# Optimization experiments

Measured on AMD Instinct MI355X. Metric: run time of the kernel, lower is better.

## Reference

```python
import jax, jax.numpy as jnp
import numpy as np

C_MSA, C_PAIR, C = 64, 128, 32


def setup_inputs() -> dict:
    key = jax.random.key(0)
    ks = jax.random.split(key, 7)
    n_msa, n_token = 512, 384
    msa = jax.random.normal(ks[0], (n_msa, n_token, C_MSA), dtype=jnp.float32)
    gamma = jnp.ones((C_MSA,), dtype=jnp.float32)
    beta = jnp.zeros((C_MSA,), dtype=jnp.float32)
    # nn.Linear weights are [out, in]
    w_a = jax.random.normal(ks[1], (C, C_MSA), dtype=jnp.float32) * (1.0 / np.sqrt(C_MSA))
    w_b = jax.random.normal(ks[2], (C, C_MSA), dtype=jnp.float32) * (1.0 / np.sqrt(C_MSA))
    w_out = jax.random.normal(ks[3], (C_PAIR, C * C), dtype=jnp.float32) * (1.0 / np.sqrt(C * C))
    b_out = jax.random.normal(ks[4], (C_PAIR,), dtype=jnp.float32) * 0.01
    return {"msa": msa, "gamma": gamma, "beta": beta, "w_a": w_a, "w_b": w_b,
            "w_out": w_out, "b_out": b_out}


def _layernorm(x, gamma, beta, eps=1e-5):
    mu = jnp.mean(x, axis=-1, keepdims=True)
    var = jnp.mean(jnp.square(x - mu), axis=-1, keepdims=True)
    return (x - mu) * jax.lax.rsqrt(var + eps) * gamma + beta


def reference(msa, gamma, beta, w_a, w_b, w_out, b_out):
    # msa: [S, I, c_msa]
    n_msa = msa.shape[0]
    m = _layernorm(msa, gamma, beta)
    a = jnp.einsum('sic,dc->sid', m, w_a)  # [S, I, C]
    b = jnp.einsum('sic,dc->sid', m, w_b)  # [S, I, C]
    # outer product mean over MSA dim as a single GEMM-style contraction
    o = jnp.einsum('sic,sjd->ijcd', a, b) / n_msa  # [I, J, C, C]
    n_token = o.shape[0]
    o_flat = o.reshape(n_token, n_token, C * C)
    z = jnp.einsum('ijk,pk->ijp', o_flat, w_out) + b_out  # [I, J, c_pair]
    return z
```

## Files before the change

kernel.cpp:

```cpp
#include <hip/hip_runtime.h>
#include <hip/hip_bf16.h>
#include <stdint.h>

#define S_DIM 512
#define I_DIM 384
#define CMSA  64
#define CDIM  32
#define M_DIM (I_DIM*CDIM)
#define P_DIM 128

typedef __attribute__((ext_vector_type(8))) short  s16x8;
typedef __attribute__((ext_vector_type(8))) __bf16 bf16x8;
typedef __attribute__((ext_vector_type(4))) float  f32x4;

static __device__ __forceinline__ unsigned short f2bf(float f) {
  union { float f; unsigned u; } v; v.f = f;
  unsigned r = v.u + 0x7FFFu + ((v.u >> 16) & 1u);
  return (unsigned short)(r >> 16);
}

static __device__ __forceinline__ void gload_lds16(const void* g, void* l) {
  __builtin_amdgcn_global_load_lds(
      (__attribute__((address_space(1))) void*)(g),
      (__attribute__((address_space(3))) void*)(l), 16, 0, 0);
}

__global__ __launch_bounds__(256) void ln_proj_kernel(
    const float* __restrict__ msa, const float* __restrict__ gamma,
    const float* __restrict__ beta, const float* __restrict__ w_a,
    const float* __restrict__ w_b, unsigned short* __restrict__ Ag,
    unsigned short* __restrict__ Bg)
{
  __shared__ float wl[2][32][64];
  __shared__ float gb[2][64];
  __shared__ unsigned short atr[2][32][64];

  const int tid = threadIdx.x;
  float* wflat = &wl[0][0][0];
  for (int t = tid; t < 2048; t += 256) { wflat[t] = w_a[t]; wflat[2048 + t] = w_b[t]; }
  if (tid < 64) { gb[0][tid] = gamma[tid]; gb[1][tid] = beta[tid]; }
  __syncthreads();

  const int q = tid & 3, sl = tid >> 2;
  const int s = blockIdx.x * 64 + sl;
  const int i = blockIdx.y;
  const float* row = msa + ((size_t)s * I_DIM + i) * CMSA + q * 16;

  float x[16];
  #pragma unroll
  for (int u = 0; u < 4; ++u) {
    float4 v = *(const float4*)(row + 4*u);
    x[4*u] = v.x; x[4*u+1] = v.y; x[4*u+2] = v.z; x[4*u+3] = v.w;
  }
  float sum = 0.f, sq = 0.f;
  #pragma unroll
  for (int j = 0; j < 16; ++j) { sum += x[j]; sq += x[j]*x[j]; }
  sum += __shfl_xor(sum, 1); sum += __shfl_xor(sum, 2);
  sq  += __shfl_xor(sq, 1);  sq  += __shfl_xor(sq, 2);
  const float mean = sum * (1.f/64.f);
  const float var  = sq  * (1.f/64.f) - mean*mean;
  const float rstd = rsqrtf(var + 1e-5f);
  float m[16];
  #pragma unroll
  for (int j = 0; j < 16; ++j)
    m[j] = (x[j] - mean) * rstd * gb[0][q*16+j] + gb[1][q*16+j];

  for (int c = 0; c < 32; ++c) {
    float pa = 0.f, pb = 0.f;
    #pragma unroll
    for (int u = 0; u < 4; ++u) {
      float4 wa = *(const float4*)&wl[0][c][q*16 + 4*u];
      float4 wb = *(const float4*)&wl[1][c][q*16 + 4*u];
      pa += m[4*u]*wa.x + m[4*u+1]*wa.y + m[4*u+2]*wa.z + m[4*u+3]*wa.w;
      pb += m[4*u]*wb.x + m[4*u+1]*wb.y + m[4*u+2]*wb.z + m[4*u+3]*wb.w;
    }
    pa += __shfl_xor(pa, 1); pa += __shfl_xor(pa, 2);
    pb += __shfl_xor(pb, 1); pb += __shfl_xor(pb, 2);
    if (q == 0) {
      atr[0][c][sl] = f2bf(pa * (1.f/512.f));
      atr[1][c][sl] = f2bf(pb);
    }
  }
  __syncthreads();
  const int c2 = tid >> 3, su = (tid & 7) * 8;
  const size_t gbase = ((size_t)i * CDIM + c2) * S_DIM + (size_t)blockIdx.x * 64 + su;
  *(s16x8*)(Ag + gbase) = *(const s16x8*)&atr[0][c2][su];
  *(s16x8*)(Bg + gbase) = *(const s16x8*)&atr[1][c2][su];
}

__global__ __launch_bounds__(256) void wconv_kernel(
    const float* __restrict__ w, unsigned short* __restrict__ wp)
{
  const int idx = blockIdx.x * 256 + threadIdx.x;
  const int p = idx >> 10, k = idx & 1023;
  const int c = k >> 5, d = k & 31;
  wp[p*1024 + d*32 + c] = f2bf(w[idx]);
}

__global__ __launch_bounds__(512, 2) void opm_gemm_kernel(
    const unsigned short* __restrict__ Ag, const unsigned short* __restrict__ Bg,
    const unsigned short* __restrict__ Wp, const float* __restrict__ b_out,
    float* __restrict__ z)
{
  __shared__ __align__(16) unsigned char lds[131072];

  const int tid = threadIdx.x;
  const int l = tid & 63, w = tid >> 6;
  const int wr = w >> 2, wc = w & 3;

  const int bid = blockIdx.x;
  const int xcd = bid & 7, local = bid >> 3;
  const int bn = local / 6;
  const int bm = xcd * 6 + (local % 6);

  const unsigned short* pA[4];
  const unsigned short* pB[4];
  int u16[4];
  #pragma unroll
  for (int it = 0; it < 4; ++it) {
    const int u = it*512 + tid;
    const int r = u >> 3, slot = u & 7;
    const int ks8 = slot ^ (r & 7);
    pA[it] = Ag + ((size_t)(bm*256 + r))*S_DIM + ks8*8;
    pB[it] = Bg + ((size_t)(bn*256 + r))*S_DIM + ks8*8;
    u16[it] = u * 16;
  }

  int a_base[8], b_base[4];
  #pragma unroll
  for (int mi = 0; mi < 8; ++mi) {
    const int rowA = wr*128 + mi*16 + (l & 15);
    a_base[mi] = rowA*128 + ((((l >> 4)) ^ (rowA & 7)) << 4);
  }
  #pragma unroll
  for (int ni = 0; ni < 4; ++ni) {
    const int rowB = wc*64 + ni*16 + (l & 15);
    b_base[ni] = 65536 + rowB*128 + ((((l >> 4)) ^ (rowB & 7)) << 4);
  }

  f32x4 acc[8][4];
  #pragma unroll
  for (int a = 0; a < 8; ++a)
    #pragma unroll
    for (int b = 0; b < 4; ++b)
      acc[a][b] = (f32x4){0.f, 0.f, 0.f, 0.f};

  #pragma unroll
  for (int it = 0; it < 4; ++it) {
    gload_lds16(pA[it], lds + u16[it]);
    gload_lds16(pB[it], lds + 65536 + u16[it]);
    pA[it] += 64; pB[it] += 64;
  }
  __syncthreads();

  int cur = 0;
  for (int kt = 0; kt < 8; ++kt) {
    if (kt < 7) {
      const int nb = (cur ^ 1) * 32768;
      #pragma unroll
      for (int it = 0; it < 4; ++it) {
        gload_lds16(pA[it], lds + nb + u16[it]);
        gload_lds16(pB[it], lds + 65536 + nb + u16[it]);
        pA[it] += 64; pB[it] += 64;
      }
    }
    const int cb = cur * 32768;
    #pragma unroll
    for (int ks = 0; ks < 2; ++ks) {
      bf16x8 af[8], bf[4];
      const int kx = ks << 6;
      #pragma unroll
      for (int mi = 0; mi < 8; ++mi)
        af[mi] = *(const bf16x8*)(lds + cb + (a_base[mi] ^ kx));
      #pragma unroll
      for (int ni = 0; ni < 4; ++ni)
        bf[ni] = *(const bf16x8*)(lds + cb + (b_base[ni] ^ kx));
      __builtin_amdgcn_s_setprio(1);
      #pragma unroll
      for (int mi = 0; mi < 8; ++mi)
        #pragma unroll
        for (int ni = 0; ni < 4; ++ni)
          acc[mi][ni] = __builtin_amdgcn_mfma_f32_16x16x32_bf16(
              af[mi], bf[ni], acc[mi][ni], 0, 0, 0);
      __builtin_amdgcn_s_setprio(0);
    }
    __syncthreads();
    cur ^= 1;
  }

  #pragma unroll
  for (int mi = 0; mi < 8; ++mi) {
    const int iloc = wr*4 + (mi >> 1);
    const int cb2 = (mi & 1)*16 + (l >> 4)*4;
    #pragma unroll
    for (int ni = 0; ni < 4; ++ni) {
      const int jloc = wc*2 + (ni >> 1);
      const int d = (ni & 1)*16 + (l & 15);
      const int pair = iloc*8 + jloc;
      #pragma unroll
      for (int rp = 0; rp < 2; ++rp) {
        const int kp = d*32 + cb2 + 2*rp;
        int byte = pair*2048 + kp*2;
        byte ^= ((pair & 7) << 4) ^ (((byte >> 7) & 7) << 4);
        unsigned int val = (unsigned int)f2bf(acc[mi][ni][2*rp])
                         | ((unsigned int)f2bf(acc[mi][ni][2*rp+1]) << 16);
        *(unsigned int*)(lds + byte) = val;
      }
    }
  }
  __syncthreads();

  const unsigned short* wrow = Wp + ((size_t)(w*16 + (l & 15)))*1024 + (l >> 4)*8;
  f32x4 accz[4];
  #pragma unroll
  for (int ni = 0; ni < 4; ++ni) accz[ni] = (f32x4){0.f,0.f,0.f,0.f};

  #pragma unroll 4
  for (int ksp = 0; ksp < 32; ++ksp) {
    const bf16x8 wf = *(const bf16x8*)(wrow + ksp*32);
    const int kbyte = ksp*64 + (l >> 4)*16;
    const int kswz = ((kbyte >> 7) & 7) << 4;
    #pragma unroll
    for (int ni = 0; ni < 4; ++ni) {
      const int pair = ni*16 + (l & 15);
      int byte = pair*2048 + kbyte;
      byte ^= ((pair & 7) << 4) ^ kswz;
      const bf16x8 of = *(const bf16x8*)(lds + byte);
      accz[ni] = __builtin_amdgcn_mfma_f32_16x16x32_bf16(wf, of, accz[ni], 0, 0, 0);
    }
  }

  const int p0 = w*16 + (l >> 4)*4;
  const float4 bo = *(const float4*)(b_out + p0);
  #pragma unroll
  for (int ni = 0; ni < 4; ++ni) {
    const int pair = ni*16 + (l & 15);
    const int gi = bm*8 + (pair >> 3), gj = bn*8 + (pair & 7);
    float4 v;
    v.x = accz[ni][0] + bo.x; v.y = accz[ni][1] + bo.y;
    v.z = accz[ni][2] + bo.z; v.w = accz[ni][3] + bo.w;
    *(float4*)(z + ((size_t)gi * I_DIM + gj) * P_DIM + p0) = v;
  }
}

extern "C" void kernel_launch(void* const* d_in, const int* in_sizes, int n_in,
                              void* d_out, int out_size, void* d_ws, size_t ws_size,
                              hipStream_t stream) {
  const float* msa   = (const float*)d_in[0];
  const float* gamma = (const float*)d_in[1];
  const float* beta  = (const float*)d_in[2];
  const float* w_a   = (const float*)d_in[3];
  const float* w_b   = (const float*)d_in[4];
  const float* w_out = (const float*)d_in[5];
  const float* b_out = (const float*)d_in[6];
  float* z = (float*)d_out;

  unsigned short* Ag = (unsigned short*)d_ws;
  unsigned short* Bg = Ag + (size_t)M_DIM * S_DIM;
  unsigned short* Wp = Bg + (size_t)M_DIM * S_DIM;

  hipLaunchKernelGGL(ln_proj_kernel, dim3(8, 384), dim3(256), 0, stream,
                     msa, gamma, beta, w_a, w_b, Ag, Bg);
  hipLaunchKernelGGL(wconv_kernel, dim3(512), dim3(256), 0, stream, w_out, Wp);
  hipLaunchKernelGGL(opm_gemm_kernel, dim3(2304), dim3(512), 0, stream,
                     Ag, Bg, Wp, b_out, z);
}
```

Before: 369.0 us.

## Restructure LN-projection kernel and split GEMM prefetch with explicit vmcnt waits

The layernorm/projection kernel is rewritten so that each lane holds one output channel's weight row in registers. Each wave processes rows with a full-wave shuffle reduction, and results are packed as bf16 pairs into a swizzled LDS transpose buffer before vectorized stores. This avoids the LDS weight staging and the 32-iteration serial loop over channels. In the GEMM main loop, the next tile's global-to-LDS loads are split into two halves issued around the first k-substep. Explicit s_waitcnt vmcnt and raw barriers replace __syncthreads so loads overlap MFMA work, at the cost of extra barriers per iteration.

```diff
diff --git a/kernel.cpp b/kernel.cpp
--- a/kernel.cpp
+++ b/kernel.cpp
@@ -25,67 +25,84 @@
       (__attribute__((address_space(3))) void*)(l), 16, 0, 0);
 }
 
+#define VMCNT4() asm volatile("s_waitcnt vmcnt(4)" ::: "memory")
+#define VMCNT0() asm volatile("s_waitcnt vmcnt(0)" ::: "memory")
+#define BAR()    do { __builtin_amdgcn_s_barrier(); asm volatile("" ::: "memory"); } while (0)
+
 __global__ __launch_bounds__(256) void ln_proj_kernel(
     const float* __restrict__ msa, const float* __restrict__ gamma,
     const float* __restrict__ beta, const float* __restrict__ w_a,
     const float* __restrict__ w_b, unsigned short* __restrict__ Ag,
     unsigned short* __restrict__ Bg)
 {
-  __shared__ float wl[2][32][64];
-  __shared__ float gb[2][64];
-  __shared__ unsigned short atr[2][32][64];
+  __shared__ float mraw[4][64];
+  __shared__ unsigned int atr[64][32];
 
   const int tid = threadIdx.x;
-  float* wflat = &wl[0][0][0];
-  for (int t = tid; t < 2048; t += 256) { wflat[t] = w_a[t]; wflat[2048 + t] = w_b[t]; }
-  if (tid < 64) { gb[0][tid] = gamma[tid]; gb[1][tid] = beta[tid]; }
+  const int l = tid & 63, w = tid >> 6;
+  const int c = l & 31, h = l >> 5;
+  const int i = blockIdx.y;
+  const int s0 = blockIdx.x * 64;
+
+  float wa[32], wb[32];
+  #pragma unroll
+  for (int j = 0; j < 8; ++j) {
+    float4 va = *(const float4*)(w_a + c*64 + h*32 + j*4);
+    float4 vb = *(const float4*)(w_b + c*64 + h*32 + j*4);
+    wa[j*4+0] = va.x*(1.f/512.f); wa[j*4+1] = va.y*(1.f/512.f);
+    wa[j*4+2] = va.z*(1.f/512.f); wa[j*4+3] = va.w*(1.f/512.f);
+    wb[j*4+0] = vb.x; wb[j*4+1] = vb.y; wb[j*4+2] = vb.z; wb[j*4+3] = vb.w;
+  }
+  const float gam = gamma[l], bet = beta[l];
+
+  const int srow_base = s0 + w*16;
+  for (int tp = 0; tp < 8; ++tp) {
+    float resa[2], resb[2];
+    #pragma unroll
+    for (int t = 0; t < 2; ++t) {
+      const int s = srow_base + tp*2 + t;
+      const float x = msa[((size_t)s * I_DIM + i) * CMSA + l];
+      float sum = x, sq = x*x;
+      #pragma unroll
+      for (int d = 1; d < 64; d <<= 1) {
+        sum += __shfl_xor(sum, d);
+        sq  += __shfl_xor(sq, d);
+      }
+      const float mu = sum * (1.f/64.f);
+      const float rstd = rsqrtf(sq*(1.f/64.f) - mu*mu + 1e-5f);
+      const float mn = (x - mu) * rstd * gam + bet;
+      mraw[w][l] = mn;
+      float ta = 0.f, tb = 0.f;
+      #pragma unroll
+      for (int j = 0; j < 8; ++j) {
+        float4 mv = *(const float4*)&mraw[w][h*32 + j*4];
+        ta += mv.x*wa[j*4+0] + mv.y*wa[j*4+1] + mv.z*wa[j*4+2] + mv.w*wa[j*4+3];
+        tb += mv.x*wb[j*4+0] + mv.y*wb[j*4+1] + mv.z*wb[j*4+2] + mv.w*wb[j*4+3];
+      }
+      ta += __shfl_xor(ta, 32);
+      tb += __shfl_xor(tb, 32);
+      resa[t] = ta; resb[t] = tb;
+    }
+    const float v0 = h ? resb[0] : resa[0];
+    const float v1 = h ? resb[1] : resa[1];
+    const unsigned int pk = (unsigned int)f2bf(v0) | ((unsigned int)f2bf(v1) << 16);
+    const int row = c*2 + h;
+    const int sp = w*8 + tp;
+    atr[row][sp ^ (row & 31)] = pk;
+  }
   __syncthreads();
 
-  const int q = tid & 3, sl = tid >> 2;
-  const int s = blockIdx.x * 64 + sl;
-  const int i = blockIdx.y;
-  const float* row = msa + ((size_t)s * I_DIM + i) * CMSA + q * 16;
-
-  float x[16];
-  #pragma unroll
-  for (int u = 0; u < 4; ++u) {
-    float4 v = *(const float4*)(row + 4*u);
-    x[4*u] = v.x; x[4*u+1] = v.y; x[4*u+2] = v.z; x[4*u+3] = v.w;
-  }
-  float sum = 0.f, sq = 0.f;
-  #pragma unroll
-  for (int j = 0; j < 16; ++j) { sum += x[j]; sq += x[j]*x[j]; }
-  sum += __shfl_xor(sum, 1); sum += __shfl_xor(sum, 2);
-  sq  += __shfl_xor(sq, 1);  sq  += __shfl_xor(sq, 2);
-  const float mean = sum * (1.f/64.f);
-  const float var  = sq  * (1.f/64.f) - mean*mean;
-  const float rstd = rsqrtf(var + 1e-5f);
-  float m[16];
-  #pragma unroll
-  for (int j = 0; j < 16; ++j)
-    m[j] = (x[j] - mean) * rstd * gb[0][q*16+j] + gb[1][q*16+j];
-
-  for (int c = 0; c < 32; ++c) {
-    float pa = 0.f, pb = 0.f;
-    #pragma unroll
-    for (int u = 0; u < 4; ++u) {
-      float4 wa = *(const float4*)&wl[0][c][q*16 + 4*u];
-      float4 wb = *(const float4*)&wl[1][c][q*16 + 4*u];
-      pa += m[4*u]*wa.x + m[4*u+1]*wa.y + m[4*u+2]*wa.z + m[4*u+3]*wa.w;
-      pb += m[4*u]*wb.x + m[4*u+1]*wb.y + m[4*u+2]*wb.z + m[4*u+3]*wb.w;
-    }
-    pa += __shfl_xor(pa, 1); pa += __shfl_xor(pa, 2);
-    pb += __shfl_xor(pb, 1); pb += __shfl_xor(pb, 2);
-    if (q == 0) {
-      atr[0][c][sl] = f2bf(pa * (1.f/512.f));
-      atr[1][c][sl] = f2bf(pb);
-    }
-  }
-  __syncthreads();
-  const int c2 = tid >> 3, su = (tid & 7) * 8;
-  const size_t gbase = ((size_t)i * CDIM + c2) * S_DIM + (size_t)blockIdx.x * 64 + su;
-  *(s16x8*)(Ag + gbase) = *(const s16x8*)&atr[0][c2][su];
-  *(s16x8*)(Bg + gbase) = *(const s16x8*)&atr[1][c2][su];
+  const int row = tid >> 2, sp0 = (tid & 3) * 8;
+  const int oc = row >> 1, ab = row & 1;
+  unsigned int dw[8];
+  #pragma unroll
+  for (int j = 0; j < 8; ++j) dw[j] = atr[row][(sp0 + j) ^ (row & 31)];
+  unsigned short* dst = (ab ? Bg : Ag) + ((size_t)i*CDIM + oc)*S_DIM + s0 + sp0*2;
+  uint4 u0, u1;
+  u0.x = dw[0]; u0.y = dw[1]; u0.z = dw[2]; u0.w = dw[3];
+  u1.x = dw[4]; u1.y = dw[5]; u1.z = dw[6]; u1.w = dw[7];
+  *(uint4*)(dst)     = u0;
+  *(uint4*)(dst + 8) = u1;
 }
 
 __global__ __launch_bounds__(256) void wconv_kernel(
@@ -93,8 +110,8 @@
 {
   const int idx = blockIdx.x * 256 + threadIdx.x;
   const int p = idx >> 10, k = idx & 1023;
-  const int c = k >> 5, d = k & 31;
-  wp[p*1024 + d*32 + c] = f2bf(w[idx]);
+  const int cc = k >> 5, d = k & 31;
+  wp[p*1024 + d*32 + cc] = f2bf(w[idx]);
 }
 
 __global__ __launch_bounds__(512, 2) void opm_gemm_kernel(
@@ -151,20 +168,22 @@
     gload_lds16(pB[it], lds + 65536 + u16[it]);
     pA[it] += 64; pB[it] += 64;
   }
-  __syncthreads();
 
   int cur = 0;
   for (int kt = 0; kt < 8; ++kt) {
+    const int cb = cur * 32768;
+    const int nb = (cur ^ 1) * 32768;
     if (kt < 7) {
-      const int nb = (cur ^ 1) * 32768;
-      #pragma unroll
-      for (int it = 0; it < 4; ++it) {
+      #pragma unroll
+      for (int it = 0; it < 2; ++it) {
         gload_lds16(pA[it], lds + nb + u16[it]);
         gload_lds16(pB[it], lds + 65536 + nb + u16[it]);
-        pA[it] += 64; pB[it] += 64;
-      }
-    }
-    const int cb = cur * 32768;
+      }
+      VMCNT4();
+    } else {
+      VMCNT0();
+    }
+    BAR();
     #pragma unroll
     for (int ks = 0; ks < 2; ++ks) {
       bf16x8 af[8], bf[4];
@@ -183,8 +202,22 @@
           acc[mi][ni] = __builtin_amdgcn_mfma_f32_16x16x32_bf16(
               af[mi], bf[ni], acc[mi][ni], 0, 0, 0);
       __builtin_amdgcn_s_setprio(0);
-    }
-    __syncthreads();
+      if (ks == 0) {
+        if (kt < 7) {
+          #pragma unroll
+          for (int it = 2; it < 4; ++it) {
+            gload_lds16(pA[it], lds + nb + u16[it]);
+            gload_lds16(pB[it], lds + 65536 + nb + u16[it]);
+          }
+        }
+        BAR();
+      }
+    }
+    if (kt < 7) {
+      #pragma unroll
+      for (int it = 0; it < 4; ++it) { pA[it] += 64; pB[it] += 64; }
+    }
+    BAR();
     cur ^= 1;
   }
 
```

Measured after the change: 386.0 us. +4.6%, slower.

## Switch OPM GEMM main loop to 3-stage pipeline with K=32 tiles and vmcnt waits

Applied to the files above, without the earlier changes.

Restructures the GEMM K loop from two buffers of 64-wide K tiles into three rotating buffers of 32-wide K tiles. Loads are issued two stages ahead, and the loop waits with explicit s_waitcnt vmcnt plus a raw s_barrier instead of a full __syncthreads drain. The XOR swizzle on LDS reads is dropped in favour of a plain 64-byte row layout. The goal is more latency hiding and fewer full drains, at the cost of twice as many barriers, less MFMA work per barrier, and possible LDS bank conflicts without the swizzle.

```diff
diff --git a/kernel.cpp b/kernel.cpp
--- a/kernel.cpp
+++ b/kernel.cpp
@@ -24,6 +24,10 @@
       (__attribute__((address_space(1))) void*)(g),
       (__attribute__((address_space(3))) void*)(l), 16, 0, 0);
 }
+
+#define VMCNT4() asm volatile("s_waitcnt vmcnt(4)" ::: "memory")
+#define VMCNT0() asm volatile("s_waitcnt vmcnt(0)" ::: "memory")
+#define BAR()    do { __builtin_amdgcn_s_barrier(); asm volatile("" ::: "memory"); } while (0)
 
 __global__ __launch_bounds__(256) void ln_proj_kernel(
     const float* __restrict__ msa, const float* __restrict__ gamma,
@@ -93,8 +97,8 @@
 {
   const int idx = blockIdx.x * 256 + threadIdx.x;
   const int p = idx >> 10, k = idx & 1023;
-  const int c = k >> 5, d = k & 31;
-  wp[p*1024 + d*32 + c] = f2bf(w[idx]);
+  const int cc = k >> 5, d = k & 31;
+  wp[p*1024 + d*32 + cc] = f2bf(w[idx]);
 }
 
 __global__ __launch_bounds__(512, 2) void opm_gemm_kernel(
@@ -113,29 +117,20 @@
   const int bn = local / 6;
   const int bm = xcd * 6 + (local % 6);
 
-  const unsigned short* pA[4];
-  const unsigned short* pB[4];
-  int u16[4];
-  #pragma unroll
-  for (int it = 0; it < 4; ++it) {
-    const int u = it*512 + tid;
-    const int r = u >> 3, slot = u & 7;
-    const int ks8 = slot ^ (r & 7);
-    pA[it] = Ag + ((size_t)(bm*256 + r))*S_DIM + ks8*8;
-    pB[it] = Bg + ((size_t)(bn*256 + r))*S_DIM + ks8*8;
-    u16[it] = u * 16;
-  }
-
-  int a_base[8], b_base[4];
+  const unsigned short* a_src = Ag + ((size_t)(bm*256 + (tid >> 2)))*S_DIM + (tid & 3)*8;
+  const unsigned short* b_src = Bg + ((size_t)(bn*256 + (tid >> 2)))*S_DIM + (tid & 3)*8;
+  const int dst0 = tid * 16;
+
+  int a_off[8], b_off[4];
   #pragma unroll
   for (int mi = 0; mi < 8; ++mi) {
     const int rowA = wr*128 + mi*16 + (l & 15);
-    a_base[mi] = rowA*128 + ((((l >> 4)) ^ (rowA & 7)) << 4);
+    a_off[mi] = rowA*64 + ((l >> 4) * 16);
   }
   #pragma unroll
   for (int ni = 0; ni < 4; ++ni) {
     const int rowB = wc*64 + ni*16 + (l & 15);
-    b_base[ni] = 65536 + rowB*128 + ((((l >> 4)) ^ (rowB & 7)) << 4);
+    b_off[ni] = 16384 + rowB*64 + ((l >> 4) * 16);
   }
 
   f32x4 acc[8][4];
@@ -145,47 +140,45 @@
     for (int b = 0; b < 4; ++b)
       acc[a][b] = (f32x4){0.f, 0.f, 0.f, 0.f};
 
-  #pragma unroll
-  for (int it = 0; it < 4; ++it) {
-    gload_lds16(pA[it], lds + u16[it]);
-    gload_lds16(pB[it], lds + 65536 + u16[it]);
-    pA[it] += 64; pB[it] += 64;
-  }
-  __syncthreads();
-
-  int cur = 0;
-  for (int kt = 0; kt < 8; ++kt) {
-    if (kt < 7) {
-      const int nb = (cur ^ 1) * 32768;
-      #pragma unroll
-      for (int it = 0; it < 4; ++it) {
-        gload_lds16(pA[it], lds + nb + u16[it]);
-        gload_lds16(pB[it], lds + 65536 + nb + u16[it]);
-        pA[it] += 64; pB[it] += 64;
-      }
-    }
-    const int cb = cur * 32768;
-    #pragma unroll
-    for (int ks = 0; ks < 2; ++ks) {
-      bf16x8 af[8], bf[4];
-      const int kx = ks << 6;
-      #pragma unroll
-      for (int mi = 0; mi < 8; ++mi)
-        af[mi] = *(const bf16x8*)(lds + cb + (a_base[mi] ^ kx));
+  #define STAGE(kt, bb) do {                                                  \
+    const unsigned short* as_ = a_src + (kt)*32;                              \
+    const unsigned short* bs_ = b_src + (kt)*32;                              \
+    unsigned char* lb_ = lds + (bb)*32768;                                    \
+    gload_lds16(as_,             lb_ + dst0);                                 \
+    gload_lds16(as_ + 128*S_DIM, lb_ + dst0 + 8192);                          \
+    gload_lds16(bs_,             lb_ + 16384 + dst0);                         \
+    gload_lds16(bs_ + 128*S_DIM, lb_ + 16384 + dst0 + 8192);                  \
+  } while (0)
+
+  STAGE(0, 0);
+  STAGE(1, 1);
+  VMCNT4();
+  BAR();
+
+  int cb = 0, sb = 2;
+  for (int t = 0; t < 16; ++t) {
+    if (t < 14) STAGE(t + 2, sb);
+    const int base = cb * 32768;
+    bf16x8 af[8], bf[4];
+    #pragma unroll
+    for (int mi = 0; mi < 8; ++mi)
+      af[mi] = *(const bf16x8*)(lds + base + a_off[mi]);
+    #pragma unroll
+    for (int ni = 0; ni < 4; ++ni)
+      bf[ni] = *(const bf16x8*)(lds + base + b_off[ni]);
+    __builtin_amdgcn_s_setprio(1);
+    #pragma unroll
+    for (int mi = 0; mi < 8; ++mi)
       #pragma unroll
       for (int ni = 0; ni < 4; ++ni)
-        bf[ni] = *(const bf16x8*)(lds + cb + (b_base[ni] ^ kx));
-      __builtin_amdgcn_s_setprio(1);
-      #pragma unroll
-      for (int mi = 0; mi < 8; ++mi)
-        #pragma unroll
-        for (int ni = 0; ni < 4; ++ni)
-          acc[mi][ni] = __builtin_amdgcn_mfma_f32_16x16x32_bf16(
-              af[mi], bf[ni], acc[mi][ni], 0, 0, 0);
-      __builtin_amdgcn_s_setprio(0);
-    }
-    __syncthreads();
-    cur ^= 1;
+        acc[mi][ni] = __builtin_amdgcn_mfma_f32_16x16x32_bf16(
+            af[mi], bf[ni], acc[mi][ni], 0, 0, 0);
+    __builtin_amdgcn_s_setprio(0);
+    if (t < 14)       VMCNT4();
+    else if (t == 14) VMCNT0();
+    BAR();
+    cb = (cb == 2) ? 0 : cb + 1;
+    sb = (sb == 2) ? 0 : sb + 1;
   }
 
   #pragma unroll
```

Result: slower. 377.2 us (+2.2%).
